# Optimization experiments

Hardware: AMD Instinct MI355X
Metric: run time of the kernel (lower is better)

Reference implementation:

```python
import jax, jax.numpy as jnp
import numpy as np

B, S, H, DH = 2, 2048, 24, 32
E = H * DH  # 768


def setup_inputs() -> dict:
    key = jax.random.key(0)
    ks = jax.random.split(key, 7)
    embedding = jax.random.normal(ks[0], (B, S, E), dtype=jnp.float32)
    mask = jax.random.randint(ks[1], (B, S, S), 0, 2).astype(bool)
    # per-head QKV weights (applied as x @ W, equivalent param to torch Linear W.T)
    Wq = jax.random.normal(ks[2], (H, DH, DH), dtype=jnp.float32) * 0.05
    Wk = jax.random.normal(ks[3], (H, DH, DH), dtype=jnp.float32) * 0.05
    Wv = jax.random.normal(ks[4], (H, DH, DH), dtype=jnp.float32) * 0.05
    Wo = jax.random.normal(ks[5], (E, E), dtype=jnp.float32) * 0.02
    bo = jax.random.normal(ks[6], (E,), dtype=jnp.float32) * 0.02
    return {"embedding": embedding, "mask": mask, "Wq": Wq, "Wk": Wk,
            "Wv": Wv, "Wo": Wo, "bo": bo}


def reference(embedding, mask, Wq, Wk, Wv, Wo, bo):
    # split channels into heads: [B,S,H,DH]
    xh = embedding.reshape(B, S, H, DH)
    # per-head projections (batched over heads)
    Q = jnp.einsum('bshd,hde->bhse', xh, Wq)
    K = jnp.einsum('bshd,hde->bhse', xh, Wk)
    V = jnp.einsum('bshd,hde->bhse', xh, Wv)
    scale = 1.0 / jnp.sqrt(jnp.float32(DH))
    scores = jnp.einsum('bhqd,bhkd->bhqk', Q, K) * scale
    # faithful quirk: masked positions set to -1e-6 (not -inf)
    scores = jnp.where(mask[:, None, :, :], scores, jnp.float32(-1e-6))
    probs = jax.nn.softmax(scores, axis=-1)
    out = jnp.einsum('bhqk,bhkd->bqhd', probs, V)  # [B,S,H,DH]
    out = out.reshape(B, S, E)  # concat heads along feature dim
    return out @ Wo.T + bo
```

## Files before the change

### kernel.cpp

```cpp
#include <hip/hip_runtime.h>
#include <hip/hip_bf16.h>

#define B_  2
#define S_  2048
#define H_  24
#define DH_ 32
#define E_  768
#define SW_ (S_/32)

#define NB_QKV  ((S_/64)*(B_*H_))
#define NB_MSK4 ((B_*S_*S_)/1024)
#define NB_WO   ((E_*E_)/1024)

typedef __attribute__((ext_vector_type(8))) short short8;
typedef __attribute__((ext_vector_type(4))) float f32x4;
typedef _Float16 half8  __attribute__((ext_vector_type(8)));
typedef _Float16 half2v __attribute__((ext_vector_type(2)));
typedef __fp16   fp16x2 __attribute__((ext_vector_type(2)));

static __device__ __forceinline__ half2v cvt2h(float a, float b) {
    fp16x2 t = __builtin_amdgcn_cvt_pkrtz(a, b);
    return __builtin_bit_cast(half2v, t);
}

static __device__ __forceinline__ short4 pack4(float a, float b, float c, float d) {
    union { __hip_bfloat162 h[2]; short4 s; } u;
    u.h[0] = __float22bfloat162_rn(make_float2(a, b));
    u.h[1] = __float22bfloat162_rn(make_float2(c, d));
    return u.s;
}
static __device__ __forceinline__ short8 pack8f(const float* a, const float* b) {
    union { __hip_bfloat162 h[4]; short8 s; } u;
    u.h[0] = __float22bfloat162_rn(make_float2(a[0], a[1]));
    u.h[1] = __float22bfloat162_rn(make_float2(a[2], a[3]));
    u.h[2] = __float22bfloat162_rn(make_float2(b[0], b[1]));
    u.h[3] = __float22bfloat162_rn(make_float2(b[2], b[3]));
    return u.s;
}
static __device__ __forceinline__ short8 pack8(float4 a, float4 b) {
    union { __hip_bfloat162 h[4]; short8 s; } u;
    u.h[0] = __float22bfloat162_rn(make_float2(a.x, a.y));
    u.h[1] = __float22bfloat162_rn(make_float2(a.z, a.w));
    u.h[2] = __float22bfloat162_rn(make_float2(b.x, b.y));
    u.h[3] = __float22bfloat162_rn(make_float2(b.z, b.w));
    return u.s;
}
static __device__ __forceinline__ short8 wfrag(const float* __restrict__ Wb,
                                               int quad, int eo) {
    float w[8];
#pragma unroll
    for (int j = 0; j < 8; ++j) w[j] = Wb[(quad * 8 + j) * 32 + eo];
    return pack8f(w, w + 4);
}

#define QSCALE  0.25503487f

static __device__ __forceinline__ float mexp2(float s, unsigned mw, int pos) {
    const int m = __builtin_amdgcn_sbfe((int)mw, pos, 1);
    const int xi = __builtin_bit_cast(int, s) & m;
    return __builtin_amdgcn_exp2f(__builtin_bit_cast(float, xi));
}

__global__ __launch_bounds__(256) void prep_qkv_kernel(
    const float* __restrict__ x, const int* __restrict__ mask,
    const float* __restrict__ Wo,
    const float* __restrict__ Wq, const float* __restrict__ Wk,
    const float* __restrict__ Wv,
    __hip_bfloat16* __restrict__ Qo,
    __hip_bfloat16* __restrict__ Ko,
    _Float16* __restrict__ Vto,
    unsigned int* __restrict__ mbits, _Float16* __restrict__ Wob)
{
    const int bx = blockIdx.x;
    if (bx < NB_QKV) {
        const int bh   = bx >> 5;
        const int b    = bh / H_;
        const int h    = bh - b * H_;
        const int wave = threadIdx.x >> 6;
        const int lane = threadIdx.x & 63;
        const int col  = lane & 15;
        const int quad = lane >> 4;
        const int sw   = (bx & 31) * 64 + wave * 16;
        const int s    = sw + col;

        const float* xp = x + ((size_t)b * S_ + s) * E_ + h * DH_ + quad * 8;
        const float4 xa = *reinterpret_cast<const float4*>(xp);
        const float4 xb = *reinterpret_cast<const float4*>(xp + 4);
        const short8 xf = pack8(xa, xb);

        const int wb = h * DH_ * DH_;
        const short8 aQ0 = wfrag(Wq + wb, quad, col);
        const short8 aQ1 = wfrag(Wq + wb, quad, col + 16);
        const short8 aK0 = wfrag(Wk + wb, quad, col);
        const short8 aK1 = wfrag(Wk + wb, quad, col + 16);
        const short8 bV0 = wfrag(Wv + wb, quad, col);
        const short8 bV1 = wfrag(Wv + wb, quad, col + 16);

        const f32x4 z = {0.f, 0.f, 0.f, 0.f};
        const f32x4 qt0 = __builtin_amdgcn_mfma_f32_16x16x32_bf16(aQ0, xf, z, 0, 0, 0);
        const f32x4 qt1 = __builtin_amdgcn_mfma_f32_16x16x32_bf16(aQ1, xf, z, 0, 0, 0);
        const f32x4 kt0 = __builtin_amdgcn_mfma_f32_16x16x32_bf16(aK0, xf, z, 0, 0, 0);
        const f32x4 kt1 = __builtin_amdgcn_mfma_f32_16x16x32_bf16(aK1, xf, z, 0, 0, 0);
        const f32x4 vv0 = __builtin_amdgcn_mfma_f32_16x16x32_bf16(xf, bV0, z, 0, 0, 0);
        const f32x4 vv1 = __builtin_amdgcn_mfma_f32_16x16x32_bf16(xf, bV1, z, 0, 0, 0);

        __hip_bfloat16* qrow = Qo + ((size_t)bh * S_ + s) * DH_;
        *reinterpret_cast<short4*>(qrow + quad * 4) =
            pack4(qt0[0] * QSCALE, qt0[1] * QSCALE, qt0[2] * QSCALE, qt0[3] * QSCALE);
        *reinterpret_cast<short4*>(qrow + 16 + quad * 4) =
            pack4(qt1[0] * QSCALE, qt1[1] * QSCALE, qt1[2] * QSCALE, qt1[3] * QSCALE);

        const int t32  = s & 31;
        const int slot = (s & ~31) | (((t32 >> 2) & 1) << 4)
                       | (((t32 >> 3) << 2) | (t32 & 3));
        __hip_bfloat16* krow = Ko + ((size_t)bh * S_ + slot) * DH_;
        *reinterpret_cast<short4*>(krow + quad * 4)      = pack4(kt0[0], kt0[1], kt0[2], kt0[3]);
        *reinterpret_cast<short4*>(krow + 16 + quad * 4) = pack4(kt1[0], kt1[1], kt1[2], kt1[3]);

        const int sb = sw + quad * 4;
        union { half2v h[2]; uint2 u; } v0u, v1u;
        v0u.h[0] = cvt2h(vv0[0], vv0[1]); v0u.h[1] = cvt2h(vv0[2], vv0[3]);
        v1u.h[0] = cvt2h(vv1[0], vv1[1]); v1u.h[1] = cvt2h(vv1[2], vv1[3]);
        *reinterpret_cast<uint2*>(Vto + ((size_t)bh * DH_ + col) * S_ + sb)      = v0u.u;
        *reinterpret_cast<uint2*>(Vto + ((size_t)bh * DH_ + 16 + col) * S_ + sb) = v1u.u;
    } else if (bx < NB_QKV + NB_MSK4) {
        const int wid  = (bx - NB_QKV) * 4 + (threadIdx.x >> 6);
        const int lane = threadIdx.x & 63;
        const int rg   = wid >> 5;
        const int kc   = wid & 31;
        const int row0 = rg * 4;
        const int k    = kc * 64 + lane;
        int mv[4];
#pragma unroll
        for (int j = 0; j < 4; ++j)
            mv[j] = mask[(size_t)(row0 + j) * S_ + k];
#pragma unroll
        for (int j = 0; j < 4; ++j) {
            const unsigned long long bal = __ballot(mv[j] != 0);
            if (lane == 0) {
                uint2 w;
                w.x = (unsigned int)(bal & 0xffffffffull);
                w.y = (unsigned int)(bal >> 32);
                *reinterpret_cast<uint2*>(
                    mbits + (size_t)(row0 + j) * SW_ + kc * 2) = w;
            }
        }
    } else {
        const int i = ((bx - NB_QKV - NB_MSK4) * 256 + threadIdx.x) * 4;
        const float4 w = *reinterpret_cast<const float4*>(Wo + i);
        union { half2v h[2]; uint2 u; } uu;
        uu.h[0] = cvt2h(w.x, w.y);
        uu.h[1] = cvt2h(w.z, w.w);
        *reinterpret_cast<uint2*>(Wob + i) = uu.u;
    }
}

__global__ __launch_bounds__(64, 3) void attn_kernel(
    const __hip_bfloat16* __restrict__ Q,
    const __hip_bfloat16* __restrict__ K,
    const _Float16* __restrict__ Vt,
    const unsigned int* __restrict__ mbits,
    _Float16* __restrict__ Opart,
    float* __restrict__ lpart,
    int parts)
{
    const int bid  = blockIdx.x;
    const int xcd  = bid & 7;
    const int t_   = bid >> 3;
    const int bh   = xcd * 6 + (t_ % 6);
    const int rest = t_ / 6;
    const int qsub = rest & 31;
    const int part = rest >> 5;

    const int b    = bh / H_;
    const int h    = bh - b * H_;
    const int niter = S_ / (64 * parts);
    const int kbeg  = part * (S_ / parts);
    const int lane = threadIdx.x & 63;
    const int col  = lane & 15;
    const int quad = lane >> 4;
    const int q0   = qsub * 64;

    const __hip_bfloat16* Qbh = Q  + (size_t)bh * S_ * DH_;
    const __hip_bfloat16* Kbh = K  + (size_t)bh * S_ * DH_;
    const _Float16*       Vbh = Vt + (size_t)bh * DH_ * S_;

    short8 qf[4];
#pragma unroll
    for (int t = 0; t < 4; ++t)
        qf[t] = *reinterpret_cast<const short8*>(
            Qbh + (size_t)(q0 + t * 16 + col) * DH_ + quad * 8);

    const _Float16* Vp0 = Vbh + (size_t)col * S_ + kbeg + quad * 8;
    const _Float16* Vp1 = Vbh + (size_t)(16 + col) * S_ + kbeg + quad * 8;

    const __hip_bfloat16* Kf = Kbh + (size_t)(kbeg + col) * DH_ + quad * 8;
    const unsigned int* mbb = mbits + (size_t)b * S_ * SW_ + (kbeg >> 5);
    const unsigned int* mf0 = mbb + (size_t)(q0 +  0 + col) * SW_;
    const unsigned int* mf1 = mbb + (size_t)(q0 + 16 + col) * SW_;
    const unsigned int* mf2 = mbb + (size_t)(q0 + 32 + col) * SW_;
    const unsigned int* mf3 = mbb + (size_t)(q0 + 48 + col) * SW_;

    const int posL = quad * 8;
    const int posH = quad * 8 + 4;

    union { uint4 u; half8 v; } onesu;
    onesu.u = make_uint4(0x3C003C00u, 0x3C003C00u, 0x3C003C00u, 0x3C003C00u);
    const half8 ones_h = onesu.v;

    f32x4 o0a[4], o1a[4], la[4];
#pragma unroll
    for (int t = 0; t < 4; ++t) {
        o0a[t] = (f32x4){0.f,0.f,0.f,0.f};
        o1a[t] = (f32x4){0.f,0.f,0.f,0.f};
        la[t]  = (f32x4){0.f,0.f,0.f,0.f};
    }

    short8 ak0, ak1, ak2, ak3; uint2 am0, am1, am2, am3;
    short8 bk0, bk1, bk2, bk3; uint2 bm0, bm1, bm2, bm3;

    auto load_a = [&]() {
        ak0 = *reinterpret_cast<const short8*>(Kf);
        ak1 = *reinterpret_cast<const short8*>(Kf + 16 * DH_);
        ak2 = *reinterpret_cast<const short8*>(Kf + 32 * DH_);
        ak3 = *reinterpret_cast<const short8*>(Kf + 48 * DH_);
        am0 = *reinterpret_cast<const uint2*>(mf0);
        am1 = *reinterpret_cast<const uint2*>(mf1);
        am2 = *reinterpret_cast<const uint2*>(mf2);
        am3 = *reinterpret_cast<const uint2*>(mf3);
        Kf += 64 * DH_; mf0 += 2; mf1 += 2; mf2 += 2; mf3 += 2;
    };
    auto load_b = [&]() {
        bk0 = *reinterpret_cast<const short8*>(Kf);
        bk1 = *reinterpret_cast<const short8*>(Kf + 16 * DH_);
        bk2 = *reinterpret_cast<const short8*>(Kf + 32 * DH_);
        bk3 = *reinterpret_cast<const short8*>(Kf + 48 * DH_);
        bm0 = *reinterpret_cast<const uint2*>(mf0);
        bm1 = *reinterpret_cast<const uint2*>(mf1);
        bm2 = *reinterpret_cast<const uint2*>(mf2);
        bm3 = *reinterpret_cast<const uint2*>(mf3);
        Kf += 64 * DH_; mf0 += 2; mf1 += 2; mf2 += 2; mf3 += 2;
    };

    auto compute = [&](const short8& kA0, const short8& kA1,
                       const short8& kB0, const short8& kB1,
                       uint2 w0, uint2 w1, uint2 w2, uint2 w3) {
        const half8 vA0 = *reinterpret_cast<const half8*>(Vp0);
        const half8 vA1 = *reinterpret_cast<const half8*>(Vp1);
        const half8 vB0 = *reinterpret_cast<const half8*>(Vp0 + 32);
        const half8 vB1 = *reinterpret_cast<const half8*>(Vp1 + 32);
        const uint2 mw[4] = {w0, w1, w2, w3};
        const f32x4 z = {0.f, 0.f, 0.f, 0.f};

        f32x4 s0[4], s1[4];
#pragma unroll
        for (int t = 0; t < 4; ++t) {
            s0[t] = __builtin_amdgcn_mfma_f32_16x16x32_bf16(kA0, qf[t], z, 0, 0, 0);
            s1[t] = __builtin_amdgcn_mfma_f32_16x16x32_bf16(kA1, qf[t], z, 0, 0, 0);
        }
#pragma unroll
        for (int t = 0; t < 4; ++t) {
            float p0[4], p1[4];
#pragma unroll
            for (int r = 0; r < 4; ++r) {
                p0[r] = mexp2(s0[t][r], mw[t].x, posL + r);
                p1[r] = mexp2(s1[t][r], mw[t].x, posH + r);
            }
            union { half2v h[4]; half8 v; } pu;
            pu.h[0] = cvt2h(p0[0], p0[1]);
            pu.h[1] = cvt2h(p0[2], p0[3]);
            pu.h[2] = cvt2h(p1[0], p1[1]);
            pu.h[3] = cvt2h(p1[2], p1[3]);
            const half8 pf = pu.v;
            o0a[t] = __builtin_amdgcn_mfma_f32_16x16x32_f16(vA0, pf, o0a[t], 0, 0, 0);
            o1a[t] = __builtin_amdgcn_mfma_f32_16x16x32_f16(vA1, pf, o1a[t], 0, 0, 0);
            la[t]  = __builtin_amdgcn_mfma_f32_16x16x32_f16(ones_h, pf, la[t], 0, 0, 0);
        }

#pragma unroll
        for (int t = 0; t < 4; ++t) {
            s0[t] = __builtin_amdgcn_mfma_f32_16x16x32_bf16(kB0, qf[t], z, 0, 0, 0);
            s1[t] = __builtin_amdgcn_mfma_f32_16x16x32_bf16(kB1, qf[t], z, 0, 0, 0);
        }
#pragma unroll
        for (int t = 0; t < 4; ++t) {
            float p0[4], p1[4];
#pragma unroll
            for (int r = 0; r < 4; ++r) {
                p0[r] = mexp2(s0[t][r], mw[t].y, posL + r);
                p1[r] = mexp2(s1[t][r], mw[t].y, posH + r);
            }
            union { half2v h[4]; half8 v; } pu;
            pu.h[0] = cvt2h(p0[0], p0[1]);
            pu.h[1] = cvt2h(p0[2], p0[3]);
            pu.h[2] = cvt2h(p1[0], p1[1]);
            pu.h[3] = cvt2h(p1[2], p1[3]);
            const half8 pf = pu.v;
            o0a[t] = __builtin_amdgcn_mfma_f32_16x16x32_f16(vB0, pf, o0a[t], 0, 0, 0);
            o1a[t] = __builtin_amdgcn_mfma_f32_16x16x32_f16(vB1, pf, o1a[t], 0, 0, 0);
            la[t]  = __builtin_amdgcn_mfma_f32_16x16x32_f16(ones_h, pf, la[t], 0, 0, 0);
        }

        Vp0 += 64;
        Vp1 += 64;
    };

    load_a();
    for (int it = 0; it < niter; it += 2) {
        load_b();
        compute(ak0, ak1, ak2, ak3, am0, am1, am2, am3);
        load_a();
        compute(bk0, bk1, bk2, bk3, bm0, bm1, bm2, bm3);
    }

    _Float16* Ob = Opart + (size_t)part * B_ * S_ * E_;
    float* lp = lpart + (size_t)part * B_ * H_ * S_ + (size_t)bh * S_;
#pragma unroll
    for (int t = 0; t < 4; ++t) {
        union { half2v h[2]; uint2 u; } u0, u1;
        u0.h[0] = cvt2h(o0a[t][0], o0a[t][1]);
        u0.h[1] = cvt2h(o0a[t][2], o0a[t][3]);
        u1.h[0] = cvt2h(o1a[t][0], o1a[t][1]);
        u1.h[1] = cvt2h(o1a[t][2], o1a[t][3]);
        _Float16* orow = Ob + ((size_t)b * S_ + q0 + t * 16 + col) * E_ + h * DH_;
        *reinterpret_cast<uint2*>(orow + quad * 4)      = u0.u;
        *reinterpret_cast<uint2*>(orow + 16 + quad * 4) = u1.u;
        if (quad == 0) lp[q0 + t * 16 + col] = la[t][0];
    }
}

template <int PARTS>
__global__ __launch_bounds__(256) void proj_kernel(
    const _Float16* __restrict__ Opart,
    const float* __restrict__ lpart,
    const _Float16* __restrict__ Wob,
    const float* __restrict__ bo,
    float* __restrict__ out)
{
    const int wave = threadIdx.x >> 6;
    const int lane = threadIdx.x & 63;
    const int col  = lane & 15;
    const int quad = lane >> 4;
    const int m0   = blockIdx.x * 16;
    const int n0   = blockIdx.y * 256 + wave * 64;

    const int m = m0 + col;
    const int b = m / S_;
    const int s = m - b * S_;
    const float* lpb = lpart + (size_t)(b * H_) * S_ + s;
    const size_t BHS = (size_t)B_ * H_ * S_;
    const size_t BSE = (size_t)B_ * S_ * E_;

    union UA { uint4 u; half2v h[4]; half8 v; };

    f32x4 acc[4] = {{0.f,0.f,0.f,0.f},{0.f,0.f,0.f,0.f},
                    {0.f,0.f,0.f,0.f},{0.f,0.f,0.f,0.f}};

    float lA[PARTS]; UA oA[PARTS]; UA wA[4];
    float lB[PARTS]; UA oB[PARTS]; UA wB[4];

    auto load_a = [&](int k0) {
        const int h = k0 >> 5;
        const size_t aofs = (size_t)m * E_ + k0 + quad * 8;
#pragma unroll
        for (int pp = 0; pp < PARTS; ++pp) {
            lA[pp] = lpb[(size_t)pp * BHS + (size_t)h * S_];
            oA[pp].u = *reinterpret_cast<const uint4*>(
                Opart + (size_t)pp * BSE + aofs);
        }
#pragma unroll
        for (int j = 0; j < 4; ++j)
            wA[j].u = *reinterpret_cast<const uint4*>(
                Wob + (size_t)(n0 + j * 16 + col) * E_ + k0 + quad * 8);
    };
    auto load_b = [&](int k0) {
        const int h = k0 >> 5;
        const size_t aofs = (size_t)m * E_ + k0 + quad * 8;
#pragma unroll
        for (int pp = 0; pp < PARTS; ++pp) {
            lB[pp] = lpb[(size_t)pp * BHS + (size_t)h * S_];
            oB[pp].u = *reinterpret_cast<const uint4*>(
                Opart + (size_t)pp * BSE + aofs);
        }
#pragma unroll
        for (int j = 0; j < 4; ++j)
            wB[j].u = *reinterpret_cast<const uint4*>(
                Wob + (size_t)(n0 + j * 16 + col) * E_ + k0 + quad * 8);
    };
    auto comp_a = [&]() {
        float l = 0.f;
#pragma unroll
        for (int pp = 0; pp < PARTS; ++pp) l += lA[pp];
        const float linv = __builtin_amdgcn_rcpf(l);
        const half2v lv = cvt2h(linv, linv);
        UA ua = oA[0];
#pragma unroll
        for (int pp = 1; pp < PARTS; ++pp)
#pragma unroll
            for (int i = 0; i < 4; ++i) ua.h[i] += oA[pp].h[i];
#pragma unroll
        for (int i = 0; i < 4; ++i) ua.h[i] *= lv;
#pragma unroll
        for (int j = 0; j < 4; ++j)
            acc[j] = __builtin_amdgcn_mfma_f32_16x16x32_f16(ua.v, wA[j].v, acc[j], 0, 0, 0);
    };
    auto comp_b = [&]() {
        float l = 0.f;
#pragma unroll
        for (int pp = 0; pp < PARTS; ++pp) l += lB[pp];
        const float linv = __builtin_amdgcn_rcpf(l);
        const half2v lv = cvt2h(linv, linv);
        UA ua = oB[0];
#pragma unroll
        for (int pp = 1; pp < PARTS; ++pp)
#pragma unroll
            for (int i = 0; i < 4; ++i) ua.h[i] += oB[pp].h[i];
#pragma unroll
        for (int i = 0; i < 4; ++i) ua.h[i] *= lv;
#pragma unroll
        for (int j = 0; j < 4; ++j)
            acc[j] = __builtin_amdgcn_mfma_f32_16x16x32_f16(ua.v, wB[j].v, acc[j], 0, 0, 0);
    };

    load_a(0);
    for (int k0 = 0; k0 < E_; k0 += 64) {
        load_b(k0 + 32);
        comp_a();
        if (k0 + 64 < E_) load_a(k0 + 64);
        comp_b();
    }

#pragma unroll
    for (int j = 0; j < 4; ++j) {
        const int n = n0 + j * 16 + col;
        const float bias = bo[n];
#pragma unroll
        for (int r = 0; r < 4; ++r) {
            const int mm = m0 + quad * 4 + r;
            out[(size_t)mm * E_ + n] = acc[j][r] + bias;
        }
    }
}

extern "C" void kernel_launch(void* const* d_in, const int* in_sizes, int n_in,
                              void* d_out, int out_size, void* d_ws, size_t ws_size,
                              hipStream_t stream)
{
    const float* emb = (const float*)d_in[0];
    const int*   msk = (const int*)d_in[1];
    const float* Wq  = (const float*)d_in[2];
    const float* Wk  = (const float*)d_in[3];
    const float* Wv  = (const float*)d_in[4];
    const float* Wo  = (const float*)d_in[5];
    const float* bo  = (const float*)d_in[6];
    float* out = (float*)d_out;

    const size_t nqkv = (size_t)B_ * H_ * S_ * DH_;
    char* p = (char*)d_ws;
    __hip_bfloat16* Q    = (__hip_bfloat16*)p;  p += nqkv * 2;
    __hip_bfloat16* Kp   = (__hip_bfloat16*)p;  p += nqkv * 2;
    _Float16*      Vt    = (_Float16*)p;        p += nqkv * 2;
    unsigned int*  mbits = (unsigned int*)p;    p += (size_t)B_ * S_ * SW_ * 4;
    _Float16*      Wob   = (_Float16*)p;        p += (size_t)E_ * E_ * 2;
    _Float16*      Op    = (_Float16*)p;
    const size_t base = (size_t)(p - (char*)d_ws);

    const size_t per_part = (size_t)nqkv * 2 + (size_t)B_ * H_ * S_ * 4;
    int parts = 1;
    if (ws_size >= base + 4 * per_part)      parts = 4;
    else if (ws_size >= base + 2 * per_part) parts = 2;
    float* lpart = (float*)(Op + (size_t)parts * nqkv);

    prep_qkv_kernel<<<NB_QKV + NB_MSK4 + NB_WO, 256, 0, stream>>>(
        emb, msk, Wo, Wq, Wk, Wv, Q, Kp, Vt, mbits, Wob);
    attn_kernel<<<1536 * parts, 64, 0, stream>>>(
        Q, Kp, Vt, mbits, Op, lpart, parts);
    if (parts == 4)
        proj_kernel<4><<<dim3((B_ * S_) / 16, E_ / 256), 256, 0, stream>>>(
            Op, lpart, Wob, bo, out);
    else if (parts == 2)
        proj_kernel<2><<<dim3((B_ * S_) / 16, E_ / 256), 256, 0, stream>>>(
            Op, lpart, Wob, bo, out);
    else
        proj_kernel<1><<<dim3((B_ * S_) / 16, E_ / 256), 256, 0, stream>>>(
            Op, lpart, Wob, bo, out);
}
```

Baseline: 225.5 us.

## Split projection K-loop across two wave groups and cap attention split at two parts

The output projection kernel now launches 512 threads per block, and two groups of four waves each cover half of the K dimension. Partial accumulators from the second group are reduced through shared memory before the first group adds the bias and writes the output. Separately, the attention split-K is limited to at most two parts, down from four. This roughly halves the partial O/l buffers the projection must read and combine, at the cost of less parallelism in the attention kernel.

```diff
diff --git a/kernel.cpp b/kernel.cpp
--- a/kernel.cpp
+++ b/kernel.cpp
@@ -330,19 +330,23 @@
 }
 
 template <int PARTS>
-__global__ __launch_bounds__(256) void proj_kernel(
+__global__ __launch_bounds__(512, 6) void proj_kernel(
     const _Float16* __restrict__ Opart,
     const float* __restrict__ lpart,
     const _Float16* __restrict__ Wob,
     const float* __restrict__ bo,
     float* __restrict__ out)
 {
+    __shared__ float lds[4 * 64 * 20];
+
     const int wave = threadIdx.x >> 6;
     const int lane = threadIdx.x & 63;
     const int col  = lane & 15;
     const int quad = lane >> 4;
+    const int kg   = wave >> 2;
+    const int wn   = wave & 3;
     const int m0   = blockIdx.x * 16;
-    const int n0   = blockIdx.y * 256 + wave * 64;
+    const int n0   = blockIdx.y * 256 + wn * 64;
 
     const int m = m0 + col;
     const int b = m / S_;
@@ -422,22 +426,36 @@
             acc[j] = __builtin_amdgcn_mfma_f32_16x16x32_f16(ua.v, wB[j].v, acc[j], 0, 0, 0);
     };
 
-    load_a(0);
-    for (int k0 = 0; k0 < E_; k0 += 64) {
+    const int kbeg = kg * (E_ / 2);
+    const int kend = kbeg + E_ / 2;
+    load_a(kbeg);
+    for (int k0 = kbeg; k0 < kend; k0 += 64) {
         load_b(k0 + 32);
         comp_a();
-        if (k0 + 64 < E_) load_a(k0 + 64);
+        if (k0 + 64 < kend) load_a(k0 + 64);
         comp_b();
     }
 
-#pragma unroll
-    for (int j = 0; j < 4; ++j) {
-        const int n = n0 + j * 16 + col;
-        const float bias = bo[n];
-#pragma unroll
-        for (int r = 0; r < 4; ++r) {
-            const int mm = m0 + quad * 4 + r;
-            out[(size_t)mm * E_ + n] = acc[j][r] + bias;
+    if (kg == 1) {
+#pragma unroll
+        for (int j = 0; j < 4; ++j) {
+            float* lp_ = &lds[((wn * 64 + j * 16 + col) * 20) + quad * 4];
+#pragma unroll
+            for (int r = 0; r < 4; ++r) lp_[r] = acc[j][r];
+        }
+    }
+    __syncthreads();
+    if (kg == 0) {
+#pragma unroll
+        for (int j = 0; j < 4; ++j) {
+            const float* lp_ = &lds[((wn * 64 + j * 16 + col) * 20) + quad * 4];
+            const int n = n0 + j * 16 + col;
+            const float bias = bo[n];
+#pragma unroll
+            for (int r = 0; r < 4; ++r) {
+                const int mm = m0 + quad * 4 + r;
+                out[(size_t)mm * E_ + n] = acc[j][r] + lp_[r] + bias;
+            }
         }
     }
 }
@@ -467,21 +485,17 @@
 
     const size_t per_part = (size_t)nqkv * 2 + (size_t)B_ * H_ * S_ * 4;
     int parts = 1;
-    if (ws_size >= base + 4 * per_part)      parts = 4;
-    else if (ws_size >= base + 2 * per_part) parts = 2;
+    if (ws_size >= base + 2 * per_part) parts = 2;
     float* lpart = (float*)(Op + (size_t)parts * nqkv);
 
     prep_qkv_kernel<<<NB_QKV + NB_MSK4 + NB_WO, 256, 0, stream>>>(
         emb, msk, Wo, Wq, Wk, Wv, Q, Kp, Vt, mbits, Wob);
     attn_kernel<<<1536 * parts, 64, 0, stream>>>(
         Q, Kp, Vt, mbits, Op, lpart, parts);
-    if (parts == 4)
-        proj_kernel<4><<<dim3((B_ * S_) / 16, E_ / 256), 256, 0, stream>>>(
-            Op, lpart, Wob, bo, out);
-    else if (parts == 2)
-        proj_kernel<2><<<dim3((B_ * S_) / 16, E_ / 256), 256, 0, stream>>>(
+    if (parts == 2)
+        proj_kernel<2><<<dim3((B_ * S_) / 16, E_ / 256), 512, 0, stream>>>(
             Op, lpart, Wob, bo, out);
     else
-        proj_kernel<1><<<dim3((B_ * S_) / 16, E_ / 256), 256, 0, stream>>>(
+        proj_kernel<1><<<dim3((B_ * S_) / 16, E_ / 256), 512, 0, stream>>>(
             Op, lpart, Wob, bo, out);
 }
```

Measured after the change: 245.1 us. 8.7% more time.
